# Kernel optimization log

Measured on AMD Instinct MI355X. Metric: run time of the kernel, lower is better.

## Reference

```python
import jax, jax.numpy as jnp
import numpy as np

N = 50000      # nodes
E = 800000     # edges (avg in-degree ~16)
IN = 64        # in_size
OUT = 64       # out_size
DELTA = 2.83   # PNA delta ~ log(avg_degree + 1)
MOM_EPS = 1e-30
BN_EPS = 1e-5


def setup_inputs() -> dict:
    key = jax.random.key(0)
    ks = jax.random.split(key, 8)
    node_feat = jax.random.normal(ks[0], (N, IN), dtype=jnp.float32)
    # Linear M: (2*IN -> IN); store weight as (2*IN, IN) for x @ W
    Wm = jax.random.normal(ks[1], (2 * IN, IN), dtype=jnp.float32) * (1.0 / np.sqrt(2 * IN))
    bm = jnp.zeros((IN,), jnp.float32)
    # Linear U: ((4 aggs * 3 scalers + 1) * IN -> OUT) = (13*IN -> OUT)
    Wu = jax.random.normal(ks[2], (13 * IN, OUT), dtype=jnp.float32) * (1.0 / np.sqrt(13 * IN))
    bu = jnp.zeros((OUT,), jnp.float32)
    gamma = jnp.ones((OUT,), jnp.float32)
    beta = jnp.zeros((OUT,), jnp.float32)
    src = jax.random.randint(ks[3], (E,), 0, N, dtype=jnp.int32)
    dst = jax.random.randint(ks[4], (E,), 0, N, dtype=jnp.int32)
    return {"node_feat": node_feat, "Wm": Wm, "bm": bm, "Wu": Wu, "bu": bu,
            "gamma": gamma, "beta": beta, "src": src, "dst": dst}


def _pna_forward(node_feat, Wm, bm, Wu, bu, gamma, beta, src, dst):
    # message MLP: M(h_src || h_dst) computed without materializing the concat
    msg = node_feat[src] @ Wm[:IN] + node_feat[dst] @ Wm[IN:] + bm  # (E, IN)

    deg = jax.ops.segment_sum(jnp.ones((E,), msg.dtype), dst, num_segments=N)  # (N,)
    safe_deg = jnp.maximum(deg, 1.0)[:, None]
    has_nbr = (deg > 0.0)[:, None]

    # multi-statistic ragged segment reduce
    s = jax.ops.segment_sum(msg, dst, num_segments=N)
    mean = s / safe_deg
    mean_sq = jax.ops.segment_sum(msg * msg, dst, num_segments=N) / safe_deg
    var = jax.nn.relu(mean_sq - mean * mean)
    std = jnp.sqrt(var + MOM_EPS)
    mx = jnp.where(has_nbr, jax.ops.segment_max(msg, dst, num_segments=N), 0.0)
    mn = jnp.where(has_nbr, jax.ops.segment_min(msg, dst, num_segments=N), 0.0)

    h = jnp.concatenate([mean, mx, mn, std], axis=1)  # (N, 4*IN)

    # scalers: identity, amplification log(D+1)/delta, attenuation delta/log(D+1)
    logD = jnp.log(deg + 1.0)[:, None]
    safe_logD = jnp.where(logD > 0.0, logD, 1.0)  # zero-degree rows masked below
    h_all = jnp.concatenate([h, h * (safe_logD / DELTA), h * (DELTA / safe_logD)], axis=1)
    h_neigh = jnp.where(has_nbr, h_all, 0.0)  # zero-degree nodes get 0 (DGL behavior)

    # update MLP + graph size norm (single graph: snorm = 1/sqrt(N))
    z = jnp.concatenate([node_feat, h_neigh], axis=1) @ Wu + bu  # (N, OUT)
    snorm = 1.0 / jnp.sqrt(jnp.asarray(N, z.dtype))
    z = z * snorm

    # BatchNorm1d, training mode (batch stats, biased variance)
    mu = jnp.mean(z, axis=0)
    v = jnp.mean((z - mu) ** 2, axis=0)
    return (z - mu) / jnp.sqrt(v + BN_EPS) * gamma + beta


def reference(node_feat, Wm, bm, Wu, bu, gamma, beta, src, dst):
    return _pna_forward(node_feat, Wm, bm, Wu, bu, gamma, beta, src, dst)
```

## Files before the change

kernel.cpp:

```cpp
#include <hip/hip_runtime.h>
#include <hip/hip_bf16.h>


#define DELTA_C 2.83f
#define BN_EPS_C 1e-5f
#define MOM_EPS_C 1e-30f
#define FLT_BIG 3.402823466e38f
#define BSHIFT 7
#define NBMAX 512

typedef __attribute__((ext_vector_type(8))) short bf16x8;
typedef __attribute__((ext_vector_type(4))) float f32x4;

static __device__ __forceinline__ unsigned short f2bf(float f) {
    unsigned u = __float_as_uint(f);
    unsigned r = (u + 0x7FFFu + ((u >> 16) & 1u)) >> 16;
    return (unsigned short)r;
}
static __device__ __forceinline__ unsigned pack2(float a, float b) {
    return (unsigned)f2bf(a) | ((unsigned)f2bf(b) << 16);
}
static __device__ __forceinline__ float bflo(unsigned u) { return __uint_as_float(u << 16); }
static __device__ __forceinline__ float bfhi(unsigned u) { return __uint_as_float(u & 0xFFFF0000u); }

__global__ __launch_bounds__(512) void init_small(
    int* __restrict__ bcnt, float* __restrict__ bnacc)
{
    int t = threadIdx.x;
    if (t < NBMAX) bcnt[t] = 0;
    if (t < 128) bnacc[t] = 0.f;
}

__global__ __launch_bounds__(256) void repack_wu(
    const float* __restrict__ Wu, short* __restrict__ Wup)
{
    int idx = blockIdx.x * 256 + threadIdx.x;
    if (idx >= 26 * 4 * 64) return;
    int lane = idx & 63, c = (idx >> 6) & 3, kc = idx >> 8;
    int kbase = kc * 32 + (lane >> 4) * 8;
    int col = c * 16 + (lane & 15);
    unsigned short o[8];
    #pragma unroll
    for (int i = 0; i < 8; ++i)
        o[i] = f2bf(Wu[(size_t)(kbase + i) * 64 + col]);
    uint4 u;
    u.x = o[0] | ((unsigned)o[1] << 16);
    u.y = o[2] | ((unsigned)o[3] << 16);
    u.z = o[4] | ((unsigned)o[5] << 16);
    u.w = o[6] | ((unsigned)o[7] << 16);
    *(uint4*)(Wup + (size_t)idx * 8) = u;
}

__global__ __launch_bounds__(256) void proj_ab(
    const float* __restrict__ x, const float* __restrict__ Wm,
    unsigned* __restrict__ Ab, float* __restrict__ B,
    unsigned* __restrict__ xbu, int n)
{
    __shared__ float wm[128][68];
    __shared__ float xs[64][68];
    int t = threadIdx.x;
    for (int i = t; i < 2048; i += 256) {
        int k = i >> 4, c4 = (i & 15) << 2;
        *(float4*)&wm[k][c4] = *(const float4*)&Wm[k * 64 + c4];
    }
    int row0 = blockIdx.x * 64;
    for (int i = t; i < 1024; i += 256) {
        int r = i >> 4, k4 = (i & 15) << 2;
        int row = row0 + r;
        float4 v = make_float4(0.f, 0.f, 0.f, 0.f);
        if (row < n) v = *(const float4*)&x[(size_t)row * 64 + k4];
        *(float4*)&xs[r][k4] = v;
    }
    __syncthreads();
    int tr = t >> 4, tc = t & 15, c0 = tc << 2;
    float a[4][4] = {}; float b[4][4] = {};
    #pragma unroll 8
    for (int k = 0; k < 64; ++k) {
        float4 wa = *(float4*)&wm[k][c0];
        float4 wb = *(float4*)&wm[64 + k][c0];
        #pragma unroll
        for (int i = 0; i < 4; ++i) {
            float xv = xs[tr * 4 + i][k];
            a[i][0] += xv * wa.x; a[i][1] += xv * wa.y; a[i][2] += xv * wa.z; a[i][3] += xv * wa.w;
            b[i][0] += xv * wb.x; b[i][1] += xv * wb.y; b[i][2] += xv * wb.z; b[i][3] += xv * wb.w;
        }
    }
    #pragma unroll
    for (int i = 0; i < 4; ++i) {
        int r = tr * 4 + i;
        int row = row0 + r;
        uint2 xp;
        xp.x = pack2(xs[r][c0], xs[r][c0 + 1]);
        xp.y = pack2(xs[r][c0 + 2], xs[r][c0 + 3]);
        *(uint2*)&xbu[(size_t)row * 32 + (c0 >> 1)] = xp;
        if (row < n) {
            uint2 ap;
            ap.x = pack2(a[i][0], a[i][1]);
            ap.y = pack2(a[i][2], a[i][3]);
            *(uint2*)&Ab[(size_t)row * 32 + (c0 >> 1)] = ap;
            *(float4*)&B[(size_t)row * 64 + c0] = make_float4(b[i][0], b[i][1], b[i][2], b[i][3]);
        }
    }
}

__global__ __launch_bounds__(256) void bin_count(
    const int* __restrict__ dst, int* __restrict__ bcnt, int e)
{
    __shared__ int h[NBMAX];
    int t = threadIdx.x;
    for (int b = t; b < NBMAX; b += 256) h[b] = 0;
    __syncthreads();
    int base = blockIdx.x * 4096;
    int cnt = min(4096, e - base);
    for (int i = t; i < cnt; i += 256)
        atomicAdd(&h[dst[base + i] >> BSHIFT], 1);
    __syncthreads();
    for (int b = t; b < NBMAX; b += 256)
        if (h[b]) atomicAdd(&bcnt[b], h[b]);
}

__global__ void bin_scan(const int* __restrict__ bcnt, int* __restrict__ boff,
                         int* __restrict__ gcur, int nb,
                         int* __restrict__ offs, int n, int e)
{
    int t = threadIdx.x;
    int v[8]; int s = 0;
    #pragma unroll
    for (int j = 0; j < 8; ++j) {
        int b = t * 8 + j;
        v[j] = (b < nb) ? bcnt[b] : 0;
        s += v[j];
    }
    int inc = s;
    #pragma unroll
    for (int st = 1; st < 64; st <<= 1) {
        int u = __shfl_up(inc, st);
        if (t >= st) inc += u;
    }
    int ex = inc - s;
    #pragma unroll
    for (int j = 0; j < 8; ++j) {
        int b = t * 8 + j;
        if (b < nb) { boff[b] = ex; gcur[b] = ex; }
        ex += v[j];
    }
    if (t == 63) { boff[nb] = e; offs[n] = e; }
}

__global__ __launch_bounds__(256) void bin_scatter(
    const int* __restrict__ src, const int* __restrict__ dst,
    int* __restrict__ gcur, int2* __restrict__ pairs_out, int e)
{
    __shared__ int hcnt[NBMAX], hstart[NBMAX], hcur[NBMAX], gpos[NBMAX];
    __shared__ int2 pairs[4096];
    int t = threadIdx.x;
    int base = blockIdx.x * 4096;
    int cnt = min(4096, e - base);
    for (int b = t; b < NBMAX; b += 256) hcnt[b] = 0;
    __syncthreads();

    int ls[16], ld[16];
    #pragma unroll
    for (int j = 0; j < 16; ++j) {
        int i = t + j * 256;
        ls[j] = 0; ld[j] = -1;
        if (i < cnt) {
            ls[j] = src[base + i];
            ld[j] = dst[base + i];
            atomicAdd(&hcnt[ld[j] >> BSHIFT], 1);
        }
    }
    __syncthreads();
    if (t < 64) {
        int v[8]; int s = 0;
        #pragma unroll
        for (int j = 0; j < 8; ++j) { v[j] = hcnt[t * 8 + j]; s += v[j]; }
        int inc = s;
        #pragma unroll
        for (int st = 1; st < 64; st <<= 1) {
            int u = __shfl_up(inc, st);
            if (t >= st) inc += u;
        }
        int ex = inc - s;
        #pragma unroll
        for (int j = 0; j < 8; ++j) {
            hstart[t * 8 + j] = ex;
            hcur[t * 8 + j] = ex;
            ex += v[j];
        }
    }
    __syncthreads();
    #pragma unroll
    for (int j = 0; j < 16; ++j) {
        if (ld[j] >= 0) {
            int pos = atomicAdd(&hcur[ld[j] >> BSHIFT], 1);
            pairs[pos] = make_int2(ls[j], ld[j]);
        }
    }
    __syncthreads();
    for (int b = t; b < NBMAX; b += 256) {
        int c = hcnt[b];
        if (c) gpos[b] = atomicAdd(&gcur[b], c);
    }
    __syncthreads();
    #pragma unroll
    for (int j = 0; j < 16; ++j) {
        int i = t + j * 256;
        if (i < cnt) {
            int2 p = pairs[i];
            int b = p.y >> BSHIFT;
            pairs_out[gpos[b] + (i - hstart[b])] = p;
        }
    }
}

__global__ __launch_bounds__(128) void csr_fill(
    const int2* __restrict__ pairs, const int* __restrict__ boff,
    int* __restrict__ offs, int* __restrict__ csr, int n)
{
    __shared__ int hist[128], pref[128], cur[128];
    int b = blockIdx.x, t = threadIdx.x;
    int base = boff[b], cnt = boff[b + 1] - base;
    int node0 = b << BSHIFT;
    hist[t] = 0;
    __syncthreads();
    for (int i = t; i < cnt; i += 128)
        atomicAdd(&hist[pairs[base + i].y & 127], 1);
    __syncthreads();
    if (t < 64) {
        int v0 = hist[2 * t], v1 = hist[2 * t + 1];
        int s = v0 + v1, inc = s;
        #pragma unroll
        for (int st = 1; st < 64; st <<= 1) {
            int u = __shfl_up(inc, st);
            if (t >= st) inc += u;
        }
        int ex = inc - s;
        pref[2 * t] = ex;       cur[2 * t] = ex;
        pref[2 * t + 1] = ex + v0; cur[2 * t + 1] = ex + v0;
    }
    __syncthreads();
    int node = node0 + t;
    if (node < n) offs[node] = base + pref[t];
    for (int i = t; i < cnt; i += 128) {
        int2 p = pairs[base + i];
        int pos = atomicAdd(&cur[p.y & 127], 1);
        csr[base + pos] = p.x;
    }
}

__global__ __launch_bounds__(256) void node_reduce(
    const unsigned* __restrict__ Ab, const float* __restrict__ Bp,
    const float* __restrict__ bm,
    const int* __restrict__ offs, const int* __restrict__ csr,
    unsigned* __restrict__ hbu, float* __restrict__ s1, float* __restrict__ s2,
    int n, int npad)
{
    int wid = threadIdx.x >> 6;
    int lane = threadIdx.x & 63;
    int node = blockIdx.x * 4 + wid;
    if (node >= npad) return;
    unsigned* hrow = hbu + (size_t)node * 128;
    int l32 = lane & 31;
    int half = lane >> 5;
    int beg = 0, dg = 0;
    if (node < n) { beg = offs[node]; dg = offs[node + 1] - beg; }
    if (dg == 0) {
        if (half == 0) {
            hrow[l32] = 0u; hrow[32 + l32] = 0u; hrow[64 + l32] = 0u; hrow[96 + l32] = 0u;
        }
        if (lane == 0) { s1[node] = 0.f; s2[node] = 0.f; }
        return;
    }

    float s0 = 0.f, s1a = 0.f, ss0 = 0.f, ss1 = 0.f;
    float mx0 = -FLT_BIG, mx1 = -FLT_BIG, mn0 = FLT_BIG, mn1 = FLT_BIG;

#define ACC(u) { float v0 = bflo(u), v1 = bfhi(u);                          \
    s0 += v0; s1a += v1;                                                    \
    ss0 = fmaf(v0, v0, ss0); ss1 = fmaf(v1, v1, ss1);                       \
    mx0 = fmaxf(mx0, v0); mx1 = fmaxf(mx1, v1);                             \
    mn0 = fminf(mn0, v0); mn1 = fminf(mn1, v1); }

    int j = beg, end = beg + dg;
    for (; j + 7 < end; j += 8) {
        int i0 = csr[j],     i1 = csr[j + 1], i2 = csr[j + 2], i3 = csr[j + 3];
        int i4 = csr[j + 4], i5 = csr[j + 5], i6 = csr[j + 6], i7 = csr[j + 7];
        int sa = half ? i1 : i0;
        int sb = half ? i3 : i2;
        int sc = half ? i5 : i4;
        int sd = half ? i7 : i6;
        unsigned ua = Ab[(size_t)sa * 32 + l32];
        unsigned ub = Ab[(size_t)sb * 32 + l32];
        unsigned uc = Ab[(size_t)sc * 32 + l32];
        unsigned ud = Ab[(size_t)sd * 32 + l32];
        ACC(ua); ACC(ub); ACC(uc); ACC(ud);
    }
    for (; j + 3 < end; j += 4) {
        int i0 = csr[j], i1 = csr[j + 1], i2 = csr[j + 2], i3 = csr[j + 3];
        int sa = half ? i1 : i0;
        int sb = half ? i3 : i2;
        unsigned ua = Ab[(size_t)sa * 32 + l32];
        unsigned ub = Ab[(size_t)sb * 32 + l32];
        ACC(ua); ACC(ub);
    }
    for (; j + 1 < end; j += 2) {
        int i0 = csr[j], i1 = csr[j + 1];
        int sa = half ? i1 : i0;
        unsigned ua = Ab[(size_t)sa * 32 + l32];
        ACC(ua);
    }
    if (j < end) {
        int sa = csr[j];
        unsigned ua = Ab[(size_t)sa * 32 + l32];
        if (half == 0) ACC(ua);
    }
#undef ACC

    s0 += __shfl_xor(s0, 32);  s1a += __shfl_xor(s1a, 32);
    ss0 += __shfl_xor(ss0, 32); ss1 += __shfl_xor(ss1, 32);
    mx0 = fmaxf(mx0, __shfl_xor(mx0, 32)); mx1 = fmaxf(mx1, __shfl_xor(mx1, 32));
    mn0 = fminf(mn0, __shfl_xor(mn0, 32)); mn1 = fminf(mn1, __shfl_xor(mn1, 32));

    float fd = (float)dg, inv = 1.0f / fd;
    float2 bv = *(const float2*)(Bp + (size_t)node * 64 + 2 * l32);
    float2 bmv = *(const float2*)(bm + 2 * l32);
    float bn0 = bv.x + bmv.x, bn1 = bv.y + bmv.y;
    float ma0 = s0 * inv, ma1 = s1a * inv;
    float var0 = ss0 * inv - ma0 * ma0; if (var0 < 0.f) var0 = 0.f;
    float var1 = ss1 * inv - ma1 * ma1; if (var1 < 0.f) var1 = 0.f;
    float sd0 = sqrtf(var0 + MOM_EPS_C), sd1 = sqrtf(var1 + MOM_EPS_C);

    if (half == 0) {
        hrow[l32]      = pack2(ma0 + bn0, ma1 + bn1);
        hrow[32 + l32] = pack2(mx0 + bn0, mx1 + bn1);
        hrow[64 + l32] = pack2(mn0 + bn0, mn1 + bn1);
        hrow[96 + l32] = pack2(sd0, sd1);
    }
    if (lane == 0) {
        float logD = logf(fd + 1.0f);
        s1[node] = logD / DELTA_C;
        s2[node] = DELTA_C / logD;
    }
}

__global__ __launch_bounds__(256) void gemm_mfma(
    const short* __restrict__ xb, const short* __restrict__ hb,
    const float* __restrict__ s1p, const float* __restrict__ s2p,
    const short* __restrict__ Wup, const float* __restrict__ bu,
    float* __restrict__ z, float* __restrict__ bnacc, int n, float snorm)
{
    __shared__ float bnl[4][2][64];
    int t = threadIdx.x;
    int lane = t & 63, w = t >> 6;
    int rb = blockIdx.x * 128 + w * 32;
    int r16 = lane & 15, kg = lane >> 4;

    f32x4 accx[2][4] = {};
    f32x4 acc1[2][4] = {};
    f32x4 acc2[2][4] = {};
    f32x4 acc3[2][4] = {};

    const short* xr0 = xb + (size_t)(rb + r16) * 64 + kg * 8;
    const short* xr1 = xr0 + 16 * 64;

    #pragma unroll
    for (int kc = 0; kc < 2; ++kc) {
        bf16x8 a0 = *(const bf16x8*)(xr0 + kc * 32);
        bf16x8 a1 = *(const bf16x8*)(xr1 + kc * 32);
        #pragma unroll
        for (int c = 0; c < 4; ++c) {
            bf16x8 b = *(const bf16x8*)(Wup + (size_t)((kc * 4 + c) * 64 + lane) * 8);
            accx[0][c] = __builtin_amdgcn_mfma_f32_16x16x32_bf16(a0, b, accx[0][c], 0, 0, 0);
            accx[1][c] = __builtin_amdgcn_mfma_f32_16x16x32_bf16(a1, b, accx[1][c], 0, 0, 0);
        }
    }

    const short* hr0 = hb + (size_t)(rb + r16) * 256 + kg * 8;
    const short* hr1 = hr0 + 16 * 256;

    #pragma unroll 1
    for (int kh = 0; kh < 8; ++kh) {
        bf16x8 a0 = *(const bf16x8*)(hr0 + kh * 32);
        bf16x8 a1 = *(const bf16x8*)(hr1 + kh * 32);
        #pragma unroll
        for (int c = 0; c < 4; ++c) {
            bf16x8 b1 = *(const bf16x8*)(Wup + (size_t)(((2  + kh) * 4 + c) * 64 + lane) * 8);
            bf16x8 b2 = *(const bf16x8*)(Wup + (size_t)(((10 + kh) * 4 + c) * 64 + lane) * 8);
            bf16x8 b3 = *(const bf16x8*)(Wup + (size_t)(((18 + kh) * 4 + c) * 64 + lane) * 8);
            acc1[0][c] = __builtin_amdgcn_mfma_f32_16x16x32_bf16(a0, b1, acc1[0][c], 0, 0, 0);
            acc1[1][c] = __builtin_amdgcn_mfma_f32_16x16x32_bf16(a1, b1, acc1[1][c], 0, 0, 0);
            acc2[0][c] = __builtin_amdgcn_mfma_f32_16x16x32_bf16(a0, b2, acc2[0][c], 0, 0, 0);
            acc2[1][c] = __builtin_amdgcn_mfma_f32_16x16x32_bf16(a1, b2, acc2[1][c], 0, 0, 0);
            acc3[0][c] = __builtin_amdgcn_mfma_f32_16x16x32_bf16(a0, b3, acc3[0][c], 0, 0, 0);
            acc3[1][c] = __builtin_amdgcn_mfma_f32_16x16x32_bf16(a1, b3, acc3[1][c], 0, 0, 0);
        }
    }

    float cs[4] = {}, css[4] = {};
    #pragma unroll
    for (int s = 0; s < 2; ++s) {
        int r0 = rb + s * 16 + kg * 4;
        float s1v[4], s2v[4];
        #pragma unroll
        for (int r = 0; r < 4; ++r) { s1v[r] = s1p[r0 + r]; s2v[r] = s2p[r0 + r]; }
        #pragma unroll
        for (int c = 0; c < 4; ++c) {
            int col = c * 16 + r16;
            float bval = bu[col];
            #pragma unroll
            for (int r = 0; r < 4; ++r) {
                int row = r0 + r;
                if (row < n) {
                    float v = (accx[s][c][r] + acc1[s][c][r]
                            + s1v[r] * acc2[s][c][r] + s2v[r] * acc3[s][c][r] + bval) * snorm;
                    z[(size_t)row * 64 + col] = v;
                    cs[c] += v;
                    css[c] = fmaf(v, v, css[c]);
                }
            }
        }
    }
    #pragma unroll
    for (int c = 0; c < 4; ++c) {
        float a = cs[c];  a += __shfl_xor(a, 16); a += __shfl_xor(a, 32); cs[c] = a;
        float b = css[c]; b += __shfl_xor(b, 16); b += __shfl_xor(b, 32); css[c] = b;
    }
    if (lane < 16) {
        #pragma unroll
        for (int c = 0; c < 4; ++c) {
            bnl[w][0][c * 16 + lane] = cs[c];
            bnl[w][1][c * 16 + lane] = css[c];
        }
    }
    __syncthreads();
    if (t < 128) {
        int st = t >> 6, cc = t & 63;
        float tot = bnl[0][st][cc] + bnl[1][st][cc] + bnl[2][st][cc] + bnl[3][st][cc];
        atomicAdd(&bnacc[st * 64 + cc], tot);
    }
}

__global__ __launch_bounds__(256) void bn_apply(
    float* __restrict__ z, const float* __restrict__ acc,
    const float* __restrict__ gamma, const float* __restrict__ beta, int n)
{
    float inv_n = 1.0f / (float)n;
    int total = n * 64;
    for (int i = blockIdx.x * blockDim.x + threadIdx.x; i < total; i += gridDim.x * blockDim.x) {
        int c = i & 63;
        float mu = acc[c] * inv_n;
        float var = acc[64 + c] * inv_n - mu * mu;
        if (var < 0.f) var = 0.f;
        float inv = rsqrtf(var + BN_EPS_C);
        z[i] = (z[i] - mu) * inv * gamma[c] + beta[c];
    }
}

extern "C" void kernel_launch(void* const* d_in, const int* in_sizes, int n_in,
                              void* d_out, int out_size, void* d_ws, size_t ws_size,
                              hipStream_t stream)
{
    const float* x     = (const float*)d_in[0];
    const float* Wm    = (const float*)d_in[1];
    const float* bm    = (const float*)d_in[2];
    const float* Wu    = (const float*)d_in[3];
    const float* bu    = (const float*)d_in[4];
    const float* gamma = (const float*)d_in[5];
    const float* beta  = (const float*)d_in[6];
    const int*   src   = (const int*)d_in[7];
    const int*   dst   = (const int*)d_in[8];

    int n = in_sizes[0] / 64;
    int e = in_sizes[7];
    int npad = ((n + 127) / 128) * 128;
    int nb = (n + 127) >> BSHIFT;
    float* z = (float*)d_out;

    char* w = (char*)d_ws;
    size_t off = 0;
    auto take = [&](size_t bytes) -> void* {
        void* p = w + off;
        off = (off + bytes + 255) & ~(size_t)255;
        return p;
    };
    unsigned* Ab    = (unsigned*)take((size_t)npad * 32 * sizeof(unsigned));
    float*    B     = (float*)take((size_t)n * 64 * sizeof(float));
    unsigned* xbu   = (unsigned*)take((size_t)npad * 32 * sizeof(unsigned));
    unsigned* hbu   = (unsigned*)take((size_t)npad * 128 * sizeof(unsigned));
    float*    s1    = (float*)take((size_t)npad * sizeof(float));
    float*    s2    = (float*)take((size_t)npad * sizeof(float));
    short*    Wup   = (short*)take((size_t)26 * 4 * 64 * 8 * sizeof(short));
    int*      offs  = (int*)take((size_t)(n + 1) * sizeof(int));
    int*      csr   = (int*)take((size_t)e * sizeof(int));
    int2*     prs   = (int2*)take((size_t)e * sizeof(int2));
    int*      bcnt  = (int*)take((size_t)NBMAX * sizeof(int));
    int*      boff  = (int*)take((size_t)(NBMAX + 1) * sizeof(int));
    int*      gcur  = (int*)take((size_t)NBMAX * sizeof(int));
    float*    bnacc = (float*)take(128 * sizeof(float));

    (void)n_in; (void)out_size; (void)ws_size;

    int nb_rows64 = npad / 64;
    int nb_chunk = (e + 4095) / 4096;

    init_small<<<1, 512, 0, stream>>>(bcnt, bnacc);
    repack_wu<<<26, 256, 0, stream>>>(Wu, Wup);
    proj_ab<<<nb_rows64, 256, 0, stream>>>(x, Wm, Ab, B, xbu, n);
    bin_count<<<nb_chunk, 256, 0, stream>>>(dst, bcnt, e);
    bin_scan<<<1, 64, 0, stream>>>(bcnt, boff, gcur, nb, offs, n, e);
    bin_scatter<<<nb_chunk, 256, 0, stream>>>(src, dst, gcur, prs, e);
    csr_fill<<<nb, 128, 0, stream>>>(prs, boff, offs, csr, n);
    node_reduce<<<(npad + 3) / 4, 256, 0, stream>>>(Ab, B, bm, offs, csr, hbu, s1, s2, n, npad);

    float snorm = (float)(1.0 / sqrt((double)n));
    gemm_mfma<<<npad / 128, 256, 0, stream>>>((const short*)xbu, (const short*)hbu,
                                              s1, s2, Wup, bu, z, bnacc, n, snorm);

    bn_apply<<<1024, 256, 0, stream>>>(z, bnacc, gamma, beta, n);
}
```

Before: 132.4 us.

## Fuse small launches, pack edge pairs into one int, vectorize BN apply

```diff
diff --git a/kernel.cpp b/kernel.cpp
--- a/kernel.cpp
+++ b/kernel.cpp
@@ -23,19 +23,16 @@
 static __device__ __forceinline__ float bflo(unsigned u) { return __uint_as_float(u << 16); }
 static __device__ __forceinline__ float bfhi(unsigned u) { return __uint_as_float(u & 0xFFFF0000u); }
 
-__global__ __launch_bounds__(512) void init_small(
+__global__ __launch_bounds__(256) void repack_wu(
+    const float* __restrict__ Wu, short* __restrict__ Wup,
     int* __restrict__ bcnt, float* __restrict__ bnacc)
 {
     int t = threadIdx.x;
-    if (t < NBMAX) bcnt[t] = 0;
-    if (t < 128) bnacc[t] = 0.f;
-}
-
-__global__ __launch_bounds__(256) void repack_wu(
-    const float* __restrict__ Wu, short* __restrict__ Wup)
-{
-    int idx = blockIdx.x * 256 + threadIdx.x;
-    if (idx >= 26 * 4 * 64) return;
+    if (blockIdx.x == 0) {
+        bcnt[t] = 0; bcnt[t + 256] = 0;
+        if (t < 128) bnacc[t] = 0.f;
+    }
+    int idx = blockIdx.x * 256 + t;
     int lane = idx & 63, c = (idx >> 6) & 3, kc = idx >> 8;
     int kbase = kc * 32 + (lane >> 4) * 8;
     int col = c * 16 + (lane & 15);
@@ -54,10 +51,12 @@
 __global__ __launch_bounds__(256) void proj_ab(
     const float* __restrict__ x, const float* __restrict__ Wm,
     unsigned* __restrict__ Ab, float* __restrict__ B,
-    unsigned* __restrict__ xbu, int n)
+    unsigned* __restrict__ xbu, int n,
+    const int* __restrict__ dst, int* __restrict__ bcnt, int e, int nb_chunk)
 {
     __shared__ float wm[128][68];
     __shared__ float xs[64][68];
+    __shared__ int h[NBMAX];
     int t = threadIdx.x;
     for (int i = t; i < 2048; i += 256) {
         int k = i >> 4, c4 = (i & 15) << 2;
@@ -101,22 +100,18 @@
             *(float4*)&B[(size_t)row * 64 + c0] = make_float4(b[i][0], b[i][1], b[i][2], b[i][3]);
         }
     }
-}
-
-__global__ __launch_bounds__(256) void bin_count(
-    const int* __restrict__ dst, int* __restrict__ bcnt, int e)
-{
-    __shared__ int h[NBMAX];
-    int t = threadIdx.x;
-    for (int b = t; b < NBMAX; b += 256) h[b] = 0;
-    __syncthreads();
-    int base = blockIdx.x * 4096;
-    int cnt = min(4096, e - base);
-    for (int i = t; i < cnt; i += 256)
-        atomicAdd(&h[dst[base + i] >> BSHIFT], 1);
-    __syncthreads();
-    for (int b = t; b < NBMAX; b += 256)
-        if (h[b]) atomicAdd(&bcnt[b], h[b]);
+    if (blockIdx.x < nb_chunk) {
+        __syncthreads();
+        for (int bb = t; bb < NBMAX; bb += 256) h[bb] = 0;
+        __syncthreads();
+        int base = blockIdx.x * 4096;
+        int cnt = min(4096, e - base);
+        for (int i = t; i < cnt; i += 256)
+            atomicAdd(&h[dst[base + i] >> BSHIFT], 1);
+        __syncthreads();
+        for (int bb = t; bb < NBMAX; bb += 256)
+            if (h[bb]) atomicAdd(&bcnt[bb], h[bb]);
+    }
 }
 
 __global__ void bin_scan(const int* __restrict__ bcnt, int* __restrict__ boff,
@@ -149,10 +144,10 @@
 
 __global__ __launch_bounds__(256) void bin_scatter(
     const int* __restrict__ src, const int* __restrict__ dst,
-    int* __restrict__ gcur, int2* __restrict__ pairs_out, int e)
+    int* __restrict__ gcur, int* __restrict__ pairs_out, int e)
 {
     __shared__ int hcnt[NBMAX], hstart[NBMAX], hcur[NBMAX], gpos[NBMAX];
-    __shared__ int2 pairs[4096];
+    __shared__ int pairs[4096];
     int t = threadIdx.x;
     int base = blockIdx.x * 4096;
     int cnt = min(4096, e - base);
@@ -194,7 +189,7 @@
     for (int j = 0; j < 16; ++j) {
         if (ld[j] >= 0) {
             int pos = atomicAdd(&hcur[ld[j] >> BSHIFT], 1);
-            pairs[pos] = make_int2(ls[j], ld[j]);
+            pairs[pos] = (ls[j] << BSHIFT) | (ld[j] & 127);
         }
     }
     __syncthreads();
@@ -207,15 +202,20 @@
     for (int j = 0; j < 16; ++j) {
         int i = t + j * 256;
         if (i < cnt) {
-            int2 p = pairs[i];
-            int b = p.y >> BSHIFT;
-            pairs_out[gpos[b] + (i - hstart[b])] = p;
+            int p = pairs[i];
+            int lo = 0, hi = NBMAX - 1;
+            #pragma unroll
+            for (int s = 256; s > 0; s >>= 1) {
+                int mid = lo + s;
+                if (mid < NBMAX && hstart[mid] <= i) lo = mid;
+            }
+            pairs_out[gpos[lo] + (i - hstart[lo])] = p;
         }
     }
 }
 
 __global__ __launch_bounds__(128) void csr_fill(
-    const int2* __restrict__ pairs, const int* __restrict__ boff,
+    const int* __restrict__ pairs, const int* __restrict__ boff,
     int* __restrict__ offs, int* __restrict__ csr, int n)
 {
     __shared__ int hist[128], pref[128], cur[128];
@@ -225,7 +225,7 @@
     hist[t] = 0;
     __syncthreads();
     for (int i = t; i < cnt; i += 128)
-        atomicAdd(&hist[pairs[base + i].y & 127], 1);
+        atomicAdd(&hist[pairs[base + i] & 127], 1);
     __syncthreads();
     if (t < 64) {
         int v0 = hist[2 * t], v1 = hist[2 * t + 1];
@@ -243,9 +243,9 @@
     int node = node0 + t;
     if (node < n) offs[node] = base + pref[t];
     for (int i = t; i < cnt; i += 128) {
-        int2 p = pairs[base + i];
-        int pos = atomicAdd(&cur[p.y & 127], 1);
-        csr[base + pos] = p.x;
+        int p = pairs[base + i];
+        int pos = atomicAdd(&cur[p & 127], 1);
+        csr[base + pos] = p >> BSHIFT;
     }
 }
 
@@ -283,26 +283,31 @@
     mn0 = fminf(mn0, v0); mn1 = fminf(mn1, v1); }
 
     int j = beg, end = beg + dg;
+    for (; j + 15 < end; j += 16) {
+        int idx[16];
+        #pragma unroll
+        for (int k = 0; k < 16; ++k) idx[k] = csr[j + k];
+        unsigned u[8];
+        #pragma unroll
+        for (int k = 0; k < 8; ++k) {
+            int sel = half ? idx[2 * k + 1] : idx[2 * k];
+            u[k] = Ab[(size_t)sel * 32 + l32];
+        }
+        #pragma unroll
+        for (int k = 0; k < 8; ++k) ACC(u[k]);
+    }
     for (; j + 7 < end; j += 8) {
-        int i0 = csr[j],     i1 = csr[j + 1], i2 = csr[j + 2], i3 = csr[j + 3];
-        int i4 = csr[j + 4], i5 = csr[j + 5], i6 = csr[j + 6], i7 = csr[j + 7];
-        int sa = half ? i1 : i0;
-        int sb = half ? i3 : i2;
-        int sc = half ? i5 : i4;
-        int sd = half ? i7 : i6;
-        unsigned ua = Ab[(size_t)sa * 32 + l32];
-        unsigned ub = Ab[(size_t)sb * 32 + l32];
-        unsigned uc = Ab[(size_t)sc * 32 + l32];
-        unsigned ud = Ab[(size_t)sd * 32 + l32];
-        ACC(ua); ACC(ub); ACC(uc); ACC(ud);
-    }
-    for (; j + 3 < end; j += 4) {
-        int i0 = csr[j], i1 = csr[j + 1], i2 = csr[j + 2], i3 = csr[j + 3];
-        int sa = half ? i1 : i0;
-        int sb = half ? i3 : i2;
-        unsigned ua = Ab[(size_t)sa * 32 + l32];
-        unsigned ub = Ab[(size_t)sb * 32 + l32];
-        ACC(ua); ACC(ub);
+        int idx[8];
+        #pragma unroll
+        for (int k = 0; k < 8; ++k) idx[k] = csr[j + k];
+        unsigned u[4];
+        #pragma unroll
+        for (int k = 0; k < 4; ++k) {
+            int sel = half ? idx[2 * k + 1] : idx[2 * k];
+            u[k] = Ab[(size_t)sel * 32 + l32];
+        }
+        #pragma unroll
+        for (int k = 0; k < 4; ++k) ACC(u[k]);
     }
     for (; j + 1 < end; j += 2) {
         int i0 = csr[j], i1 = csr[j + 1];
@@ -446,14 +451,28 @@
     const float* __restrict__ gamma, const float* __restrict__ beta, int n)
 {
     float inv_n = 1.0f / (float)n;
-    int total = n * 64;
-    for (int i = blockIdx.x * blockDim.x + threadIdx.x; i < total; i += gridDim.x * blockDim.x) {
-        int c = i & 63;
+    int tid = blockIdx.x * 256 + threadIdx.x;
+    int c0 = (tid * 4) & 63;
+    float sc[4], sh[4];
+    #pragma unroll
+    for (int k = 0; k < 4; ++k) {
+        int c = c0 + k;
         float mu = acc[c] * inv_n;
         float var = acc[64 + c] * inv_n - mu * mu;
         if (var < 0.f) var = 0.f;
-        float inv = rsqrtf(var + BN_EPS_C);
-        z[i] = (z[i] - mu) * inv * gamma[c] + beta[c];
+        float inv = rsqrtf(var + BN_EPS_C) * gamma[c];
+        sc[k] = inv;
+        sh[k] = beta[c] - mu * inv;
+    }
+    int total4 = n * 16;
+    int stride = gridDim.x * 256;
+    for (int i = tid; i < total4; i += stride) {
+        float4 v = *(float4*)&z[(size_t)i * 4];
+        v.x = fmaf(v.x, sc[0], sh[0]);
+        v.y = fmaf(v.y, sc[1], sh[1]);
+        v.z = fmaf(v.z, sc[2], sh[2]);
+        v.w = fmaf(v.w, sc[3], sh[3]);
+        *(float4*)&z[(size_t)i * 4] = v;
     }
 }
 
@@ -493,7 +512,7 @@
     short*    Wup   = (short*)take((size_t)26 * 4 * 64 * 8 * sizeof(short));
     int*      offs  = (int*)take((size_t)(n + 1) * sizeof(int));
     int*      csr   = (int*)take((size_t)e * sizeof(int));
-    int2*     prs   = (int2*)take((size_t)e * sizeof(int2));
+    int*      prs   = (int*)take((size_t)e * sizeof(int));
     int*      bcnt  = (int*)take((size_t)NBMAX * sizeof(int));
     int*      boff  = (int*)take((size_t)(NBMAX + 1) * sizeof(int));
     int*      gcur  = (int*)take((size_t)NBMAX * sizeof(int));
@@ -504,10 +523,8 @@
     int nb_rows64 = npad / 64;
     int nb_chunk = (e + 4095) / 4096;
 
-    init_small<<<1, 512, 0, stream>>>(bcnt, bnacc);
-    repack_wu<<<26, 256, 0, stream>>>(Wu, Wup);
-    proj_ab<<<nb_rows64, 256, 0, stream>>>(x, Wm, Ab, B, xbu, n);
-    bin_count<<<nb_chunk, 256, 0, stream>>>(dst, bcnt, e);
+    repack_wu<<<26, 256, 0, stream>>>(Wu, Wup, bcnt, bnacc);
+    proj_ab<<<nb_rows64, 256, 0, stream>>>(x, Wm, Ab, B, xbu, n, dst, bcnt, e, nb_chunk);
     bin_scan<<<1, 64, 0, stream>>>(bcnt, boff, gcur, nb, offs, n, e);
     bin_scatter<<<nb_chunk, 256, 0, stream>>>(src, dst, gcur, prs, e);
     csr_fill<<<nb, 128, 0, stream>>>(prs, boff, offs, csr, n);
@@ -517,5 +534,5 @@
     gemm_mfma<<<npad / 128, 256, 0, stream>>>((const short*)xbu, (const short*)hbu,
                                               s1, s2, Wup, bu, z, bnacc, n, snorm);
 
-    bn_apply<<<1024, 256, 0, stream>>>(z, bnacc, gamma, beta, n);
-}
+    bn_apply<<<512, 256, 0, stream>>>(z, bnacc, gamma, beta, n);
+}
```

Result: slower. 143.4 us (+8.3%).
